# Performance work log

Measured on AMD Instinct MI355X. Metric: run time of the kernel, lower is better.

Reference implementation:

```python
import jax, jax.numpy as jnp
import numpy as np

# model constants
D = 2048; D_INNER = 4096; H = 64; P = 64; N = 128; K = 4; CHUNK = 256
E = 8; TOPK = 2; I_EXP = 1024; I_SH = 4096
EPS = 1e-5; RES_MULT = 0.22
CONV_DIM = D_INNER + 2 * N  # n_groups=1


def rmsnorm(x, w, eps=EPS):
    var = jnp.mean(x * x, axis=-1, keepdims=True)
    return x * jax.lax.rsqrt(var + eps) * w


def segsum(x):
    # x: [..., L] -> [..., L, L] lower-triangular cumulative sums, -inf above diag
    L = x.shape[-1]
    cs = jnp.cumsum(x, axis=-1)
    d = cs[..., :, None] - cs[..., None, :]
    mask = jnp.tril(jnp.ones((L, L), dtype=bool))
    return jnp.where(mask, d, -jnp.inf)


def ssd(x, dt, A, Bm, Cm, chunk=CHUNK):
    # x:[b,s,h,p] dt:[b,s,h] A:[h] Bm/Cm:[b,s,n] (single group)
    b, S, h, p = x.shape
    n = Bm.shape[-1]
    nc = S // chunk
    xc = x.reshape(b, nc, chunk, h, p)
    dtc = dt.reshape(b, nc, chunk, h)
    Bc = Bm.reshape(b, nc, chunk, n)
    Cc = Cm.reshape(b, nc, chunk, n)
    dA = jnp.transpose(dtc * A, (0, 1, 3, 2))          # [b,c,h,l]
    dA_cum = jnp.cumsum(dA, axis=-1)                    # [b,c,h,l]
    xdt = xc * dtc[..., None]                           # [b,c,l,h,p]
    # intra-chunk (quadratic attention-like block)
    CB = jnp.einsum('bcln,bcsn->bcls', Cc, Bc)
    Lmat = jnp.exp(segsum(dA))                          # [b,c,h,l,s]
    Y = jnp.einsum('bcls,bchls,bcshp->bclhp', CB, Lmat, xdt)
    # per-chunk final states
    decay_states = jnp.exp(dA_cum[..., -1:] - dA_cum)   # [b,c,h,l]
    states = jnp.einsum('bcln,bchl,bclhp->bchpn', Bc, decay_states, xdt)
    # inter-chunk recurrence (small scan over nc chunks)
    chunk_decay = jnp.exp(dA_cum[..., -1])              # [b,c,h]
    dec_c = jnp.moveaxis(chunk_decay, 1, 0)             # [c,b,h]
    st_c = jnp.moveaxis(states, 1, 0)                   # [c,b,h,p,n]

    def step(carry, inp):
        dec, st = inp
        return carry * dec[..., None, None] + st, carry

    _, prev = jax.lax.scan(step, jnp.zeros_like(st_c[0]), (dec_c, st_c))
    prev = jnp.moveaxis(prev, 0, 1)                     # [b,c,h,p,n] state before each chunk
    out_decay = jnp.exp(jnp.transpose(dA_cum, (0, 1, 3, 2)))  # [b,c,l,h]
    Y = Y + jnp.einsum('bcln,bchpn->bclhp', Cc, prev) * out_decay[..., None]
    return Y.reshape(b, S, h, p)


def causal_conv_silu(u, w, bias):
    # u:[b,s,c], depthwise causal conv kernel w:[c,K]
    S = u.shape[1]
    up = jnp.pad(u, ((0, 0), (K - 1, 0), (0, 0)))
    y = sum(up[:, i:i + S, :] * w[:, i] for i in range(K)) + bias
    return jax.nn.silu(y)


def setup_inputs() -> dict:
    key = jax.random.key(0)
    ks = jax.random.split(key, 16)
    B, S = 1, 4096
    sc = 0.02
    return {
        'positions': jnp.arange(B * S, dtype=jnp.int32).reshape(B, S),
        'hidden_states': jax.random.normal(ks[0], (B, S, D), jnp.float32),
        'ln1_w': jnp.ones((D,), jnp.float32),
        'in_proj_w': jax.random.normal(ks[1], (D, 2 * D_INNER + 2 * N + H), jnp.float32) * sc,
        'conv_w': jax.random.normal(ks[2], (CONV_DIM, K), jnp.float32) * 0.2,
        'conv_b': jnp.zeros((CONV_DIM,), jnp.float32),
        'A_log': jnp.log(jax.random.uniform(ks[3], (H,), jnp.float32, 1.0, 16.0)),
        'dt_bias': jax.random.normal(ks[4], (H,), jnp.float32) * 0.5,
        'D_param': jnp.ones((H,), jnp.float32),
        'mamba_norm_w': jnp.ones((D_INNER,), jnp.float32),
        'out_proj_w': jax.random.normal(ks[5], (D_INNER, D), jnp.float32) * sc,
        'ln2_w': jnp.ones((D,), jnp.float32),
        'router_w': jax.random.normal(ks[6], (D, E), jnp.float32) * sc,
        'moe_w_gate_up': jax.random.normal(ks[7], (E, D, 2 * I_EXP), jnp.float32) * sc,
        'moe_w_down': jax.random.normal(ks[8], (E, I_EXP, D), jnp.float32) * sc,
        'shared_w_in': jax.random.normal(ks[9], (D, 2 * I_SH), jnp.float32) * sc,
        'shared_w_out': jax.random.normal(ks[10], (I_SH, D), jnp.float32) * sc,
    }


def reference(positions, hidden_states, ln1_w, in_proj_w, conv_w, conv_b, A_log,
              dt_bias, D_param, mamba_norm_w, out_proj_w, ln2_w, router_w,
              moe_w_gate_up, moe_w_down, shared_w_in, shared_w_out):
    B, S, _ = hidden_states.shape
    residual = hidden_states
    h = rmsnorm(hidden_states, ln1_w)
    # ---- Mamba2 mixer ----
    proj = h @ in_proj_w                                  # [B,S,2*Di+2N+H]
    z = proj[..., :D_INNER]
    xBC = proj[..., D_INNER:D_INNER + CONV_DIM]
    dt_raw = proj[..., D_INNER + CONV_DIM:]
    xBC = causal_conv_silu(xBC, conv_w, conv_b)
    x = xBC[..., :D_INNER].reshape(B, S, H, P)
    Bm = xBC[..., D_INNER:D_INNER + N]
    Cm = xBC[..., D_INNER + N:]
    dt = jax.nn.softplus(dt_raw + dt_bias)                # [B,S,H]
    A = -jnp.exp(A_log)                                   # [H]
    y = ssd(x, dt, A, Bm, Cm) + x * D_param[None, None, :, None]
    y = y.reshape(B, S, D_INNER)
    y = rmsnorm(y * jax.nn.silu(z), mamba_norm_w)         # gated RMSNorm
    mamba_out = y @ out_proj_w
    hidden = residual + mamba_out * RES_MULT
    residual = hidden
    # ---- MoE + shared MLP ----
    h2 = rmsnorm(hidden, ln2_w)
    ht = h2.reshape(-1, D)
    T = ht.shape[0]
    logits = ht @ router_w                                # [T,E]
    topv, topi = jax.lax.top_k(logits, TOPK)
    wts = jax.nn.softmax(topv, axis=-1)
    gates = jnp.zeros((T, E), ht.dtype).at[jnp.arange(T)[:, None], topi].set(wts)
    moe_out = jnp.zeros_like(ht)
    for e in range(E):
        gu = ht @ moe_w_gate_up[e]
        a = jax.nn.silu(gu[:, :I_EXP]) * gu[:, I_EXP:]
        moe_out = moe_out + gates[:, e:e + 1] * (a @ moe_w_down[e])
    gu = ht @ shared_w_in
    shared_out = (jax.nn.silu(gu[:, :I_SH]) * gu[:, I_SH:]) @ shared_w_out
    ff = (moe_out + shared_out).reshape(B, S, D)
    hidden = residual + ff * RES_MULT
    return (hidden, residual)
```

## Files before the change

kernel.cpp:

```cpp
#include <hip/hip_runtime.h>
#include <stdint.h>

typedef unsigned short u16;
typedef __attribute__((ext_vector_type(8))) __bf16 bf16x8;
typedef __attribute__((ext_vector_type(4))) float f32x4;

#define SEQ     4096
#define DMODEL  2048
#define DINNER  4096
#define NHEADS  64
#define HEADP   64
#define NSTATE  128
#define NCHUNK  16
#define CHUNKL  256
#define NPROJ   8512
#define NPROJP  8576
#define CONVDIM 4352
#define RESM    0.22f
#define MAXROWS 9216
#define MAXTILE 72

static __device__ __forceinline__ u16 f2bf(float f){
  union { float f; uint32_t u; } v; v.f = f;
  uint32_t r = v.u + 0x7fffu + ((v.u >> 16) & 1u);
  return (u16)(r >> 16);
}
static __device__ __forceinline__ float bf2f(u16 h){
  union { uint32_t u; float f; } v; v.u = ((uint32_t)h) << 16;
  return v.f;
}
static __device__ __forceinline__ float siluf(float x){ return x / (1.f + __expf(-x)); }

static __device__ __forceinline__ void gll16(const void* g, void* l) {
  __builtin_amdgcn_global_load_lds(
      (const __attribute__((address_space(1))) void*)g,
      (__attribute__((address_space(3))) void*)l, 16, 0, 0);
}

static __device__ __forceinline__ void decode_tile(
    int id, int NB, int MB, int G, int& bx, int& by)
{
  const int nwg = NB * MB;
  int sid = id;
  if (!(nwg & 7)) {
    const int cpx = nwg >> 3;
    sid = (id & 7) * cpx + (id >> 3);
  }
  const int gsz = MB * G;
  const int fullG = NB / G;
  const int fullCnt = fullG * gsz;
  if (sid < fullCnt) {
    const int grp = sid / gsz;
    const int r = sid - grp * gsz;
    const int q = r / G;
    by = q;
    bx = grp * G + (r - q * G);
  } else {
    const int rem = NB - fullG * G;
    const int r = sid - fullCnt;
    const int q = r / rem;
    by = q;
    bx = fullG * G + (r - q * rem);
  }
}

__global__ __launch_bounds__(256) void rmsnorm_kernel(
    const float* __restrict__ in, const float* __restrict__ w,
    u16* __restrict__ out, int width)
{
  const int row = blockIdx.x;
  const float* x = in + (size_t)row * width;
  float ss = 0.f;
  for (int i = threadIdx.x * 4; i < width; i += 1024) {
    float4 v = *(const float4*)&x[i];
    ss += v.x*v.x + v.y*v.y + v.z*v.z + v.w*v.w;
  }
  #pragma unroll
  for (int off = 32; off > 0; off >>= 1) ss += __shfl_down(ss, off);
  __shared__ float red[4];
  if ((threadIdx.x & 63) == 0) red[threadIdx.x >> 6] = ss;
  __syncthreads();
  const float total = red[0] + red[1] + red[2] + red[3];
  const float scale = rsqrtf(total / (float)width + 1e-5f);
  u16* o = out + (size_t)row * width;
  for (int i = threadIdx.x * 4; i < width; i += 1024) {
    float4 v = *(const float4*)&x[i];
    float4 g = *(const float4*)&w[i];
    o[i+0] = f2bf(v.x * scale * g.x);
    o[i+1] = f2bf(v.y * scale * g.y);
    o[i+2] = f2bf(v.z * scale * g.z);
    o[i+3] = f2bf(v.w * scale * g.w);
  }
}

__global__ __launch_bounds__(256) void rmsnorm_split(
    const float* __restrict__ in, const float* __restrict__ w,
    u16* __restrict__ hi, u16* __restrict__ lo, int width)
{
  const int row = blockIdx.x;
  const float* x = in + (size_t)row * width;
  float ss = 0.f;
  for (int i = threadIdx.x * 4; i < width; i += 1024) {
    float4 v = *(const float4*)&x[i];
    ss += v.x*v.x + v.y*v.y + v.z*v.z + v.w*v.w;
  }
  #pragma unroll
  for (int off = 32; off > 0; off >>= 1) ss += __shfl_down(ss, off);
  __shared__ float red[4];
  if ((threadIdx.x & 63) == 0) red[threadIdx.x >> 6] = ss;
  __syncthreads();
  const float total = red[0] + red[1] + red[2] + red[3];
  const float scale = rsqrtf(total / (float)width + 1e-5f);
  u16* oh = hi + (size_t)row * width;
  u16* ol = lo + (size_t)row * width;
  for (int i = threadIdx.x * 4; i < width; i += 1024) {
    float4 v = *(const float4*)&x[i];
    float4 g = *(const float4*)&w[i];
    #pragma unroll
    for (int q = 0; q < 4; q++) {
      const float val = ((const float*)&v)[q] * scale * ((const float*)&g)[q];
      const u16 H = f2bf(val);
      oh[i+q] = H;
      ol[i+q] = f2bf(val - bf2f(H));
    }
  }
}

__global__ __launch_bounds__(256) void wconv_t(
    const float* __restrict__ W, u16* __restrict__ Bt, int K, int N)
{
  const size_t eo = (size_t)blockIdx.z * K * N;
  W += eo; Bt += eo;
  __shared__ float t[32][33];
  const int n0 = blockIdx.x * 32, k0 = blockIdx.y * 32;
  const int tx = threadIdx.x & 31, ty = threadIdx.x >> 5;
  #pragma unroll
  for (int r = 0; r < 32; r += 8)
    t[ty + r][tx] = W[(size_t)(k0 + ty + r) * N + n0 + tx];
  __syncthreads();
  #pragma unroll
  for (int r = 0; r < 32; r += 8)
    Bt[(size_t)(n0 + ty + r) * K + k0 + tx] = f2bf(t[tx][ty + r]);
}

__global__ __launch_bounds__(256) void wconv_t_split(
    const float* __restrict__ W, u16* __restrict__ Bth, u16* __restrict__ Btl, int K, int N)
{
  __shared__ float t[32][33];
  const int n0 = blockIdx.x * 32, k0 = blockIdx.y * 32;
  const int tx = threadIdx.x & 31, ty = threadIdx.x >> 5;
  #pragma unroll
  for (int r = 0; r < 32; r += 8)
    t[ty + r][tx] = W[(size_t)(k0 + ty + r) * N + n0 + tx];
  __syncthreads();
  #pragma unroll
  for (int r = 0; r < 32; r += 8) {
    const float val = t[tx][ty + r];
    const u16 H = f2bf(val);
    const size_t idx = (size_t)(n0 + ty + r) * K + k0 + tx;
    Bth[idx] = H;
    Btl[idx] = f2bf(val - bf2f(H));
  }
}

template<int EPI>
__global__ __launch_bounds__(256, 2) void gemm_bt(
    const u16* __restrict__ A, const u16* __restrict__ Bt,
    float* __restrict__ Cf,
    int Nreal, int K, int ldc, int NB, int MB, int G)
{
  __shared__ u16 As[128 * 32];
  __shared__ u16 Bs[128 * 32];
  int bx, by; decode_tile(blockIdx.x, NB, MB, G, bx, by);
  const int tid = threadIdx.x, lane = tid & 63;
  const int wid = tid >> 6, wr = wid >> 1, wc = wid & 1;
  const int m0 = by * 128, n0 = bx * 128;
  const int fr = lane & 15, g = lane >> 4;
  const f32x4 zero = {0.f, 0.f, 0.f, 0.f};
  f32x4 acc[4][4];
  #pragma unroll
  for (int i = 0; i < 4; i++)
    #pragma unroll
    for (int j = 0; j < 4; j++) acc[i][j] = zero;
  const u16* pA = A  + (size_t)(m0 + (tid >> 2)) * K + (tid & 3) * 8;
  const u16* pB = Bt + (size_t)(n0 + (tid >> 2)) * K + (tid & 3) * 8;
  const size_t rstep = (size_t)64 * K;
  const int l0 = tid * 8;
  for (int k0 = 0; k0 < K; k0 += 32) {
    if (k0) __syncthreads();
    gll16(pA + k0,         &As[l0]);
    gll16(pA + k0 + rstep, &As[2048 + l0]);
    gll16(pB + k0,         &Bs[l0]);
    gll16(pB + k0 + rstep, &Bs[2048 + l0]);
    __syncthreads();
    bf16x8 af[4], bfr[4];
    #pragma unroll
    for (int mi = 0; mi < 4; mi++)
      af[mi] = *(const bf16x8*)&As[(wr * 64 + mi * 16 + fr) * 32 + g * 8];
    #pragma unroll
    for (int ni = 0; ni < 4; ni++)
      bfr[ni] = *(const bf16x8*)&Bs[(wc * 64 + ni * 16 + fr) * 32 + g * 8];
    #pragma unroll
    for (int mi = 0; mi < 4; mi++)
      #pragma unroll
      for (int ni = 0; ni < 4; ni++)
        acc[mi][ni] = __builtin_amdgcn_mfma_f32_16x16x32_bf16(af[mi], bfr[ni], acc[mi][ni], 0, 0, 0);
  }
  #pragma unroll
  for (int mi = 0; mi < 4; mi++) {
    #pragma unroll
    for (int ni = 0; ni < 4; ni++) {
      const int n = n0 + wc * 64 + ni * 16 + fr;
      if (n >= Nreal) continue;
      #pragma unroll
      for (int i = 0; i < 4; i++) {
        const int m = m0 + wr * 64 + mi * 16 + g * 4 + i;
        Cf[(size_t)m * ldc + n] = acc[mi][ni][i];
      }
    }
  }
}

template<int EPI>
__global__ __launch_bounds__(256, 2) void gemm_dd(
    const u16* __restrict__ Ah, const u16* __restrict__ Al,
    const u16* __restrict__ Bh, const u16* __restrict__ Bl,
    float* __restrict__ Cf, const float* __restrict__ res,
    int Nreal, int K, int ldc, float alpha, int NB, int MB, int G)
{
  __shared__ u16 Ash[128 * 32];
  __shared__ u16 Asl[128 * 32];
  __shared__ u16 Bsh[128 * 32];
  __shared__ u16 Bsl[128 * 32];
  int bx, by; decode_tile(blockIdx.x, NB, MB, G, bx, by);
  const int tid = threadIdx.x, lane = tid & 63;
  const int wid = tid >> 6, wr = wid >> 1, wc = wid & 1;
  const int m0 = by * 128, n0 = bx * 128;
  const int fr = lane & 15, g = lane >> 4;
  const f32x4 zero = {0.f, 0.f, 0.f, 0.f};
  f32x4 acc[4][4];
  #pragma unroll
  for (int i = 0; i < 4; i++)
    #pragma unroll
    for (int j = 0; j < 4; j++) acc[i][j] = zero;
  const size_t offA = (size_t)(m0 + (tid >> 2)) * K + (tid & 3) * 8;
  const size_t offB = (size_t)(n0 + (tid >> 2)) * K + (tid & 3) * 8;
  const size_t rstep = (size_t)64 * K;
  const int l0 = tid * 8;
  for (int k0 = 0; k0 < K; k0 += 32) {
    if (k0) __syncthreads();
    gll16(Ah + offA + k0,         &Ash[l0]);
    gll16(Ah + offA + k0 + rstep, &Ash[2048 + l0]);
    gll16(Al + offA + k0,         &Asl[l0]);
    gll16(Al + offA + k0 + rstep, &Asl[2048 + l0]);
    gll16(Bh + offB + k0,         &Bsh[l0]);
    gll16(Bh + offB + k0 + rstep, &Bsh[2048 + l0]);
    gll16(Bl + offB + k0,         &Bsl[l0]);
    gll16(Bl + offB + k0 + rstep, &Bsl[2048 + l0]);
    __syncthreads();
    bf16x8 ah[4], al[4], bh[4], bl[4];
    #pragma unroll
    for (int mi = 0; mi < 4; mi++) {
      const int a = (wr * 64 + mi * 16 + fr) * 32 + g * 8;
      ah[mi] = *(const bf16x8*)&Ash[a];
      al[mi] = *(const bf16x8*)&Asl[a];
    }
    #pragma unroll
    for (int ni = 0; ni < 4; ni++) {
      const int b = (wc * 64 + ni * 16 + fr) * 32 + g * 8;
      bh[ni] = *(const bf16x8*)&Bsh[b];
      bl[ni] = *(const bf16x8*)&Bsl[b];
    }
    #pragma unroll
    for (int mi = 0; mi < 4; mi++)
      #pragma unroll
      for (int ni = 0; ni < 4; ni++) {
        acc[mi][ni] = __builtin_amdgcn_mfma_f32_16x16x32_bf16(al[mi], bh[ni], acc[mi][ni], 0, 0, 0);
        acc[mi][ni] = __builtin_amdgcn_mfma_f32_16x16x32_bf16(ah[mi], bl[ni], acc[mi][ni], 0, 0, 0);
        acc[mi][ni] = __builtin_amdgcn_mfma_f32_16x16x32_bf16(ah[mi], bh[ni], acc[mi][ni], 0, 0, 0);
      }
  }
  #pragma unroll
  for (int mi = 0; mi < 4; mi++) {
    #pragma unroll
    for (int ni = 0; ni < 4; ni++) {
      const int n = n0 + wc * 64 + ni * 16 + fr;
      if (n >= Nreal) continue;
      #pragma unroll
      for (int i = 0; i < 4; i++) {
        const int m = m0 + wr * 64 + mi * 16 + g * 4 + i;
        const float v = acc[mi][ni][i];
        const size_t idx = (size_t)m * ldc + n;
        if constexpr (EPI == 1) {
          Cf[idx] = res[idx] + alpha * v;
        } else {
          Cf[idx] = v;
        }
      }
    }
  }
}

__global__ __launch_bounds__(256, 2) void gemm_moe_gu(
    const u16* __restrict__ ht, const u16* __restrict__ wGU,
    float* __restrict__ guf, const int* __restrict__ tokmap,
    const int* __restrict__ meta)
{
  const int by = blockIdx.y;
  if (by >= meta[24]) return;
  const int e = meta[32 + by];
  const int row0 = meta[104 + by];
  __shared__ u16 As[128 * 32];
  __shared__ u16 Bs[128 * 32];
  const int tid = threadIdx.x, lane = tid & 63;
  const int wid = tid >> 6, wr = wid >> 1, wc = wid & 1;
  const int n0 = blockIdx.x * 128;
  const int fr = lane & 15, g = lane >> 4;
  const f32x4 zero = {0.f, 0.f, 0.f, 0.f};
  f32x4 acc[4][4];
  #pragma unroll
  for (int i = 0; i < 4; i++)
    #pragma unroll
    for (int j = 0; j < 4; j++) acc[i][j] = zero;
  const int r4 = tid >> 2, c8 = (tid & 3) * 8;
  const int tok0 = tokmap[row0 + r4];
  const int tok1 = tokmap[row0 + 64 + r4];
  const u16* pA0 = ht + (size_t)tok0 * DMODEL + c8;
  const u16* pA1 = ht + (size_t)tok1 * DMODEL + c8;
  const u16* pB  = wGU + (size_t)e * 2048 * DMODEL + (size_t)(n0 + r4) * DMODEL + c8;
  const size_t rstep = (size_t)64 * DMODEL;
  const int l0 = tid * 8;
  for (int k0 = 0; k0 < DMODEL; k0 += 32) {
    if (k0) __syncthreads();
    gll16(pA0 + k0,        &As[l0]);
    gll16(pA1 + k0,        &As[2048 + l0]);
    gll16(pB + k0,         &Bs[l0]);
    gll16(pB + k0 + rstep, &Bs[2048 + l0]);
    __syncthreads();
    bf16x8 af[4], bfr[4];
    #pragma unroll
    for (int mi = 0; mi < 4; mi++)
      af[mi] = *(const bf16x8*)&As[(wr * 64 + mi * 16 + fr) * 32 + g * 8];
    #pragma unroll
    for (int ni = 0; ni < 4; ni++)
      bfr[ni] = *(const bf16x8*)&Bs[(wc * 64 + ni * 16 + fr) * 32 + g * 8];
    #pragma unroll
    for (int mi = 0; mi < 4; mi++)
      #pragma unroll
      for (int ni = 0; ni < 4; ni++)
        acc[mi][ni] = __builtin_amdgcn_mfma_f32_16x16x32_bf16(af[mi], bfr[ni], acc[mi][ni], 0, 0, 0);
  }
  #pragma unroll
  for (int mi = 0; mi < 4; mi++)
    #pragma unroll
    for (int ni = 0; ni < 4; ni++) {
      const int n = n0 + wc * 64 + ni * 16 + fr;
      #pragma unroll
      for (int i = 0; i < 4; i++) {
        const int m = row0 + wr * 64 + mi * 16 + g * 4 + i;
        guf[(size_t)m * 2048 + n] = acc[mi][ni][i];
      }
    }
}

__global__ __launch_bounds__(256, 2) void gemm_moe_down(
    const u16* __restrict__ abuf, const u16* __restrict__ wDN,
    u16* __restrict__ dout, const float* __restrict__ gatew,
    const int* __restrict__ meta)
{
  const int by = blockIdx.y;
  if (by >= meta[24]) return;
  const int e = meta[32 + by];
  const int row0 = meta[104 + by];
  __shared__ u16 As[128 * 32];
  __shared__ u16 Bs[128 * 32];
  const int tid = threadIdx.x, lane = tid & 63;
  const int wid = tid >> 6, wr = wid >> 1, wc = wid & 1;
  const int n0 = blockIdx.x * 128;
  const int fr = lane & 15, g = lane >> 4;
  const f32x4 zero = {0.f, 0.f, 0.f, 0.f};
  f32x4 acc[4][4];
  #pragma unroll
  for (int i = 0; i < 4; i++)
    #pragma unroll
    for (int j = 0; j < 4; j++) acc[i][j] = zero;
  const int r4 = tid >> 2, c8 = (tid & 3) * 8;
  const u16* pA = abuf + (size_t)(row0 + r4) * 1024 + c8;
  const u16* pB = wDN + (size_t)e * 1024 * 2048 + (size_t)(n0 + r4) * 1024 + c8;
  const size_t rstepA = (size_t)64 * 1024;
  const int l0 = tid * 8;
  for (int k0 = 0; k0 < 1024; k0 += 32) {
    if (k0) __syncthreads();
    gll16(pA + k0,          &As[l0]);
    gll16(pA + k0 + rstepA, &As[2048 + l0]);
    gll16(pB + k0,          &Bs[l0]);
    gll16(pB + k0 + rstepA, &Bs[2048 + l0]);
    __syncthreads();
    bf16x8 af[4], bfr[4];
    #pragma unroll
    for (int mi = 0; mi < 4; mi++)
      af[mi] = *(const bf16x8*)&As[(wr * 64 + mi * 16 + fr) * 32 + g * 8];
    #pragma unroll
    for (int ni = 0; ni < 4; ni++)
      bfr[ni] = *(const bf16x8*)&Bs[(wc * 64 + ni * 16 + fr) * 32 + g * 8];
    #pragma unroll
    for (int mi = 0; mi < 4; mi++)
      #pragma unroll
      for (int ni = 0; ni < 4; ni++)
        acc[mi][ni] = __builtin_amdgcn_mfma_f32_16x16x32_bf16(af[mi], bfr[ni], acc[mi][ni], 0, 0, 0);
  }
  #pragma unroll
  for (int mi = 0; mi < 4; mi++)
    #pragma unroll
    for (int ni = 0; ni < 4; ni++) {
      const int n = n0 + wc * 64 + ni * 16 + fr;
      #pragma unroll
      for (int i = 0; i < 4; i++) {
        const int m = row0 + wr * 64 + mi * 16 + g * 4 + i;
        dout[(size_t)m * 2048 + n] = f2bf(acc[mi][ni][i] * gatew[m]);
      }
    }
}

__global__ __launch_bounds__(256) void conv_silu_kernel(
    const float* __restrict__ proj, const float* __restrict__ cw, const float* __restrict__ cb,
    float* __restrict__ x, float* __restrict__ Bc, float* __restrict__ Cc)
{
  const int c = blockIdx.x * 256 + threadIdx.x;
  const int s = blockIdx.y;
  const float4 w = *(const float4*)&cw[c * 4];
  float acc = cb[c];
  const float* pc = proj + (size_t)DINNER + c;
  if (s >= 3) acc += pc[(size_t)(s-3) * NPROJP] * w.x;
  if (s >= 2) acc += pc[(size_t)(s-2) * NPROJP] * w.y;
  if (s >= 1) acc += pc[(size_t)(s-1) * NPROJP] * w.z;
  acc += pc[(size_t)s * NPROJP] * w.w;
  const float v = siluf(acc);
  if (c < DINNER)                 x[(size_t)s * DINNER + c] = v;
  else if (c < DINNER + NSTATE)   Bc[(size_t)s * NSTATE + (c - DINNER)] = v;
  else                            Cc[(size_t)s * NSTATE + (c - DINNER - NSTATE)] = v;
}

__global__ __launch_bounds__(256) void dt_kernel(
    const float* __restrict__ proj, const float* __restrict__ dt_bias, float* __restrict__ dt)
{
  const int i = blockIdx.x * 256 + threadIdx.x;
  const int s = i >> 6, h = i & 63;
  const float v = proj[(size_t)s * NPROJP + (DINNER + CONVDIM) + h] + dt_bias[h];
  dt[i] = fmaxf(v, 0.f) + log1pf(__expf(-fabsf(v)));
}

__global__ __launch_bounds__(64) void ssd_cum_seq(
    const float* __restrict__ dt, const float* __restrict__ A_log,
    float* __restrict__ cum, float* __restrict__ cdec)
{
  const int c = blockIdx.x, h = threadIdx.x;
  const float A = -__expf(A_log[h]);
  float run = 0.f;
  float* co = cum + ((size_t)(c * 64 + h)) * 256;
  const float* dp = dt + (size_t)c * 256 * 64 + h;
  #pragma unroll 4
  for (int l = 0; l < 256; l++) {
    run += dp[(size_t)l * 64] * A;
    co[l] = run;
  }
  cdec[c * 64 + h] = __expf(run);
}

__global__ __launch_bounds__(256) void ssd_cb(
    const float* __restrict__ Cc, const float* __restrict__ Bc, float* __restrict__ CBt)
{
  const int c = blockIdx.y;
  const int lt = blockIdx.x >> 2, st = blockIdx.x & 3;
  if (st > lt) return;
  __shared__ float Cn[128][64];
  __shared__ float Bn[128][64];
  const int tid = threadIdx.x;
  #pragma unroll
  for (int rep = 0; rep < 8; rep++) {
    const int lin = rep * 1024 + tid * 4;
    const int r = lin >> 7, cc = lin & 127;
    float4 cv = *(const float4*)&Cc[((size_t)(c*256 + lt*64 + r)) * 128 + cc];
    float4 bv = *(const float4*)&Bc[((size_t)(c*256 + st*64 + r)) * 128 + cc];
    Cn[cc+0][r] = cv.x; Cn[cc+1][r] = cv.y; Cn[cc+2][r] = cv.z; Cn[cc+3][r] = cv.w;
    Bn[cc+0][r] = bv.x; Bn[cc+1][r] = bv.y; Bn[cc+2][r] = bv.z; Bn[cc+3][r] = bv.w;
  }
  __syncthreads();
  const int lb = (tid >> 4) * 4, sb = (tid & 15) * 4;
  float acc[4][4] = {};
  for (int n = 0; n < 128; n++) {
    float cv[4], bv[4];
    #pragma unroll
    for (int i = 0; i < 4; i++) { cv[i] = Cn[n][lb+i]; bv[i] = Bn[n][sb+i]; }
    #pragma unroll
    for (int i = 0; i < 4; i++)
      #pragma unroll
      for (int j = 0; j < 4; j++) acc[i][j] += cv[i] * bv[j];
  }
  #pragma unroll
  for (int is = 0; is < 4; is++) {
    const int sg = st*64 + sb + is;
    float4 o; o.x = acc[0][is]; o.y = acc[1][is]; o.z = acc[2][is]; o.w = acc[3][is];
    *(float4*)&CBt[((size_t)(c*256 + sg)) * 256 + lt*64 + lb] = o;
  }
}

__global__ __launch_bounds__(256, 2) void ssd_intra(
    const float* __restrict__ x, const float* __restrict__ dt, const float* __restrict__ cum,
    const float* __restrict__ CBt, float* __restrict__ Yw)
{
  const int c = blockIdx.x, h = blockIdx.y, l = threadIdx.x;
  __shared__ float xs[64][64];
  __shared__ float cumL[256];
  cumL[l] = cum[((size_t)(c*64 + h)) * 256 + l];
  float Y[64];
  #pragma unroll
  for (int p = 0; p < 64; p++) Y[p] = 0.f;
  const size_t cb0 = (size_t)c * 256 * 256;
  for (int st4 = 0; st4 < 4; st4++) {
    __syncthreads();
    {
      const int j = threadIdx.x >> 2, p0 = (threadIdx.x & 3) * 16;
      const int sg = c*256 + st4*64 + j;
      const float dtv = dt[(size_t)sg * 64 + h];
      const float* xr = x + (size_t)sg * DINNER + h*64 + p0;
      #pragma unroll
      for (int q4 = 0; q4 < 4; q4++) {
        const float4 v = *(const float4*)&xr[q4*4];
        xs[j][p0 + q4*4+0] = v.x * dtv;
        xs[j][p0 + q4*4+1] = v.y * dtv;
        xs[j][p0 + q4*4+2] = v.z * dtv;
        xs[j][p0 + q4*4+3] = v.w * dtv;
      }
    }
    __syncthreads();
    if (st4 * 64 <= l) {
      const float myc = cumL[l];
      const int smax = (64 < l - st4*64 + 1) ? 64 : (l - st4*64 + 1);
      for (int s = 0; s < smax; s++) {
        const int sg = st4*64 + s;
        const float coef = CBt[cb0 + (size_t)sg*256 + l] * __expf(myc - cumL[sg]);
        const float4* xr4 = (const float4*)&xs[s][0];
        #pragma unroll
        for (int p4 = 0; p4 < 16; p4++) {
          const float4 xv = xr4[p4];
          Y[p4*4+0] += coef * xv.x;
          Y[p4*4+1] += coef * xv.y;
          Y[p4*4+2] += coef * xv.z;
          Y[p4*4+3] += coef * xv.w;
        }
      }
    }
  }
  float* yo = Yw + (size_t)(c*256 + l) * DINNER + h*64;
  #pragma unroll
  for (int p4 = 0; p4 < 16; p4++) {
    float4 o; o.x = Y[p4*4+0]; o.y = Y[p4*4+1]; o.z = Y[p4*4+2]; o.w = Y[p4*4+3];
    *(float4*)&yo[p4*4] = o;
  }
}

__global__ __launch_bounds__(256, 2) void ssd_states(
    const float* __restrict__ x, const float* __restrict__ Bc, const float* __restrict__ dt,
    const float* __restrict__ cum, float* __restrict__ states)
{
  const int c = blockIdx.x, h = blockIdx.y;
  const int p = threadIdx.x >> 2, n0 = (threadIdx.x & 3) * 32;
  __shared__ float xl[64][64];
  __shared__ float Bl[64][128];
  __shared__ float cd[256];
  {
    const int l = threadIdx.x;
    const float* cumh = cum + ((size_t)(c*64 + h)) * 256;
    cd[l] = __expf(cumh[255] - cumh[l]) * dt[(size_t)(c*256 + l) * 64 + h];
  }
  float stv[32];
  #pragma unroll
  for (int q = 0; q < 32; q++) stv[q] = 0.f;
  for (int lt = 0; lt < 4; lt++) {
    __syncthreads();
    {
      const int j = threadIdx.x >> 2, p0 = (threadIdx.x & 3) * 16;
      const int sg = c*256 + lt*64 + j;
      const float* xr = x + (size_t)sg * DINNER + h*64 + p0;
      #pragma unroll
      for (int q4 = 0; q4 < 4; q4++)
        *(float4*)&xl[j][p0 + q4*4] = *(const float4*)&xr[q4*4];
    }
    #pragma unroll
    for (int rep = 0; rep < 8; rep++) {
      const int lin = rep * 1024 + threadIdx.x * 4;
      const int r = lin >> 7, cc = lin & 127;
      *(float4*)&Bl[r][cc] = *(const float4*)&Bc[((size_t)(c*256 + lt*64 + r)) * 128 + cc];
    }
    __syncthreads();
    for (int j = 0; j < 64; j++) {
      const float v = xl[j][p] * cd[lt*64 + j];
      const float4* br = (const float4*)&Bl[j][n0];
      #pragma unroll
      for (int q4 = 0; q4 < 8; q4++) {
        const float4 bv = br[q4];
        stv[q4*4+0] += v * bv.x;
        stv[q4*4+1] += v * bv.y;
        stv[q4*4+2] += v * bv.z;
        stv[q4*4+3] += v * bv.w;
      }
    }
  }
  float* so = states + (((size_t)(c*64 + h)) * 64 + p) * 128 + n0;
  #pragma unroll
  for (int q4 = 0; q4 < 8; q4++) {
    float4 o; o.x = stv[q4*4+0]; o.y = stv[q4*4+1]; o.z = stv[q4*4+2]; o.w = stv[q4*4+3];
    *(float4*)&so[q4*4] = o;
  }
}

__global__ void ssd_scan(
    const float* __restrict__ states, const float* __restrict__ cdec, float* __restrict__ prev)
{
  const int hp = blockIdx.x;
  const int n = threadIdx.x;
  const int h = hp >> 6;
  float carry = 0.f;
  for (int c = 0; c < NCHUNK; c++) {
    const size_t idx = ((size_t)c * 4096 + hp) * 128 + n;
    prev[idx] = carry;
    carry = carry * cdec[c*64 + h] + states[idx];
  }
}

__global__ __launch_bounds__(256, 2) void ssd_final(
    const float* __restrict__ Cc, const float* __restrict__ prev, const float* __restrict__ cum,
    const float* __restrict__ x, const float* __restrict__ proj, const float* __restrict__ Dp,
    float* __restrict__ Yw)
{
  const int c = blockIdx.x, h = blockIdx.y, l = threadIdx.x;
  __shared__ float pv[64][128];
  #pragma unroll
  for (int rep = 0; rep < 8; rep++) {
    const int lin = rep * 1024 + threadIdx.x * 4;
    const int p = lin >> 7, n = lin & 127;
    *(float4*)&pv[p][n] = *(const float4*)&prev[((size_t)c * 4096 + h*64 + p) * 128 + n];
  }
  __syncthreads();
  float acc[64];
  #pragma unroll
  for (int p = 0; p < 64; p++) acc[p] = 0.f;
  const float* ccrow = Cc + (size_t)(c*256 + l) * 128;
  for (int nt = 0; nt < 4; nt++) {
    float cr[32];
    #pragma unroll
    for (int j4 = 0; j4 < 8; j4++) {
      const float4 v = *(const float4*)&ccrow[nt*32 + j4*4];
      cr[j4*4+0] = v.x; cr[j4*4+1] = v.y; cr[j4*4+2] = v.z; cr[j4*4+3] = v.w;
    }
    #pragma unroll
    for (int p = 0; p < 64; p++) {
      const float4* pvp = (const float4*)&pv[p][nt*32];
      float s = 0.f;
      #pragma unroll
      for (int j4 = 0; j4 < 8; j4++) {
        const float4 b = pvp[j4];
        s += cr[j4*4+0]*b.x + cr[j4*4+1]*b.y + cr[j4*4+2]*b.z + cr[j4*4+3]*b.w;
      }
      acc[p] += s;
    }
  }
  const float odec = __expf(cum[((size_t)(c*64 + h)) * 256 + l]);
  const float Dv = Dp[h];
  const float* xr = x + (size_t)(c*256 + l) * DINNER + h*64;
  const float* zr = proj + (size_t)(c*256 + l) * NPROJP + h*64;
  float* yo = Yw + (size_t)(c*256 + l) * DINNER + h*64;
  #pragma unroll
  for (int p = 0; p < 64; p++) {
    const float yv = yo[p] + acc[p] * odec + Dv * xr[p];
    yo[p] = yv * siluf(zr[p]);
  }
}

__global__ __launch_bounds__(256) void router_kernel(
    const float* __restrict__ h2, const float* __restrict__ ln2w,
    const float* __restrict__ rw, int* __restrict__ eidx, float* __restrict__ ew)
{
  const int t = blockIdx.x;
  const float* xr = h2 + (size_t)t * DMODEL;
  float ss = 0.f;
  for (int i = threadIdx.x; i < DMODEL; i += 256) { const float v = xr[i]; ss += v*v; }
  #pragma unroll
  for (int off = 32; off > 0; off >>= 1) ss += __shfl_down(ss, off);
  __shared__ float red[4];
  if ((threadIdx.x & 63) == 0) red[threadIdx.x >> 6] = ss;
  __syncthreads();
  const float scale = rsqrtf((red[0]+red[1]+red[2]+red[3]) / (float)DMODEL + 1e-5f);
  float acc[8];
  #pragma unroll
  for (int j = 0; j < 8; j++) acc[j] = 0.f;
  for (int i = threadIdx.x; i < DMODEL; i += 256) {
    const float v = xr[i] * scale * ln2w[i];
    const float* r = rw + (size_t)i * 8;
    #pragma unroll
    for (int j = 0; j < 8; j++) acc[j] += v * r[j];
  }
  #pragma unroll
  for (int j = 0; j < 8; j++)
    #pragma unroll
    for (int off = 32; off > 0; off >>= 1) acc[j] += __shfl_down(acc[j], off);
  __shared__ float rbuf[4][8];
  if ((threadIdx.x & 63) == 0)
    #pragma unroll
    for (int j = 0; j < 8; j++) rbuf[threadIdx.x >> 6][j] = acc[j];
  __syncthreads();
  if (threadIdx.x == 0) {
    float lg[8];
    #pragma unroll
    for (int j = 0; j < 8; j++) lg[j] = rbuf[0][j]+rbuf[1][j]+rbuf[2][j]+rbuf[3][j];
    int i1 = 0;
    #pragma unroll
    for (int j = 1; j < 8; j++) if (lg[j] > lg[i1]) i1 = j;
    int i2 = -1;
    #pragma unroll
    for (int j = 0; j < 8; j++) if (j != i1 && (i2 < 0 || lg[j] > lg[i2])) i2 = j;
    const float e2 = __expf(lg[i2] - lg[i1]);
    const float inv = 1.f / (1.f + e2);
    eidx[t*2]   = i1;  ew[t*2]   = inv;
    eidx[t*2+1] = i2;  ew[t*2+1] = e2 * inv;
  }
}

__global__ void moe_zero(int* __restrict__ tokmap, int* __restrict__ meta)
{
  const int i = blockIdx.x * 256 + threadIdx.x;
  if (i < MAXROWS) tokmap[i] = 0;
  if (i < 16) meta[i] = 0;
}

__global__ void moe_count(const int* __restrict__ eidx, int* __restrict__ meta)
{
  const int i = blockIdx.x * 256 + threadIdx.x;
  if (i < SEQ * 2) atomicAdd(&meta[eidx[i]], 1);
}

__global__ void moe_offsets(int* __restrict__ meta)
{
  if (threadIdx.x != 0 || blockIdx.x != 0) return;
  int off = 0, T = 0;
  for (int e = 0; e < 8; e++) {
    meta[16 + e] = off;
    const int nt = (meta[e] + 127) >> 7;
    for (int j = 0; j < nt; j++) {
      meta[32 + T] = e;
      meta[104 + T] = off + j * 128;
      T++;
    }
    off += nt * 128;
  }
  meta[24] = T;
}

__global__ void moe_place(
    const int* __restrict__ eidx, const float* __restrict__ ew,
    int* __restrict__ meta, int* __restrict__ tokmap,
    float* __restrict__ gatew, int* __restrict__ posmap)
{
  const int i = blockIdx.x * 256 + threadIdx.x;
  if (i >= SEQ * 2) return;
  const int e = eidx[i];
  const int pos = atomicAdd(&meta[8 + e], 1);
  const int r = meta[16 + e] + pos;
  tokmap[r] = i >> 1;
  gatew[r] = ew[i];
  posmap[i] = r;
}

__global__ __launch_bounds__(256) void glu_kernel(
    const float* __restrict__ gu, u16* __restrict__ a, int I)
{
  const int i = blockIdx.x * 256 + threadIdx.x;
  const int t = blockIdx.y;
  const float lv = gu[(size_t)t * 2 * I + i];
  const float rv = gu[(size_t)t * 2 * I + I + i];
  a[(size_t)t * I + i] = f2bf(siluf(lv) * rv);
}

__global__ __launch_bounds__(256) void final_moe(
    const float* __restrict__ h2, const float* __restrict__ shout,
    const u16* __restrict__ dout, const int* __restrict__ posmap,
    float* __restrict__ o)
{
  const int t = blockIdx.x;
  const int p0 = posmap[t*2], p1 = posmap[t*2+1];
  const u16* d0 = dout + (size_t)p0 * 2048 + threadIdx.x * 8;
  const u16* d1 = dout + (size_t)p1 * 2048 + threadIdx.x * 8;
  const size_t base = (size_t)t * 2048 + threadIdx.x * 8;
  #pragma unroll
  for (int q = 0; q < 8; q++) {
    const float ff = shout[base + q] + bf2f(d0[q]) + bf2f(d1[q]);
    o[base + q] = h2[base + q] + RESM * ff;
  }
}

#define OFF_WAH   ((size_t)0)
#define OFF_WAL   ((size_t)35127296)
#define OFF_PROJ  ((size_t)70254592)
#define OFF_X     ((size_t)210763776)
#define OFF_Y     ((size_t)277872640)
#define OFF_HP    ((size_t)344981504)
#define OFF_BC    ((size_t)378535936)
#define OFF_CC    ((size_t)380633088)
#define OFF_DT    ((size_t)382730240)
#define OFF_CUM   ((size_t)383778816)
#define OFF_CDEC  ((size_t)384827392)
#define OFF_CB    ((size_t)384831488)

extern "C" void kernel_launch(void* const* d_in, const int* in_sizes, int n_in,
                              void* d_out, int out_size, void* d_ws, size_t ws_size,
                              hipStream_t stream)
{
  const float* hs       = (const float*)d_in[1];
  const float* ln1_w    = (const float*)d_in[2];
  const float* w_inproj = (const float*)d_in[3];
  const float* conv_w   = (const float*)d_in[4];
  const float* conv_b   = (const float*)d_in[5];
  const float* A_log    = (const float*)d_in[6];
  const float* dt_bias  = (const float*)d_in[7];
  const float* D_param  = (const float*)d_in[8];
  const float* mnorm_w  = (const float*)d_in[9];
  const float* w_outp   = (const float*)d_in[10];
  const float* ln2_w    = (const float*)d_in[11];
  const float* router_w = (const float*)d_in[12];
  const float* w_gu     = (const float*)d_in[13];
  const float* w_down   = (const float*)d_in[14];
  const float* w_shin   = (const float*)d_in[15];
  const float* w_shout  = (const float*)d_in[16];

  char* ws = (char*)d_ws;
  u16*   wAh    = (u16*)(ws + OFF_WAH);
  u16*   wAl    = (u16*)(ws + OFF_WAL);
  float* projf  = (float*)(ws + OFF_PROJ);
  float* xbuf   = (float*)(ws + OFF_X);
  float* ybuf   = (float*)(ws + OFF_Y);
  float* Bcb    = (float*)(ws + OFF_BC);
  float* Ccb    = (float*)(ws + OFF_CC);
  float* dtb    = (float*)(ws + OFF_DT);
  float* cumb   = (float*)(ws + OFF_CUM);
  float* cdecb  = (float*)(ws + OFF_CDEC);
  float* cbt    = (float*)(ws + OFF_CB);

  u16*   hhi    = (u16*)(ws + OFF_HP);
  u16*   hlo    = (u16*)(ws + OFF_HP + 16777216);
  float* prevb  = (float*)(ws + OFF_HP);
  u16*   wDN    = (u16*)(ws + OFF_HP);
  float* stbuf  = (float*)(ws + OFF_WAH);
  u16*   ynhi   = (u16*)(ws + OFF_WAH);
  u16*   ynlo   = (u16*)(ws + OFF_WAL);
  u16*   wBh    = (u16*)(ws + OFF_PROJ);
  u16*   wBl    = (u16*)(ws + OFF_PROJ + 16777216);
  u16*   wE     = (u16*)(ws + OFF_WAH);
  u16*   wD     = (u16*)(ws + OFF_WAH + 33554432);
  u16*   wGU    = (u16*)(ws + OFF_WAH);
  float* guf    = (float*)(ws + OFF_PROJ);
  u16*   abufp  = (u16*)(ws + OFF_PROJ + 83886080);
  u16*   ht     = (u16*)(ws + OFF_X);
  u16*   ash    = (u16*)(ws + OFF_X + 16777216);
  u16*   dout   = (u16*)(ws + OFF_X + 16777216);
  float* shout  = (float*)(ws + OFF_Y);

  int*   eidx   = (int*)(ws + OFF_BC);
  float* ew     = (float*)(ws + OFF_BC + 65536);
  int*   posmap = (int*)(ws + OFF_BC + 131072);
  int*   tokmap = (int*)(ws + OFF_BC + 196608);
  float* gatew  = (float*)(ws + OFF_BC + 262144);
  int*   meta   = (int*)(ws + OFF_BC + 327680);

  float* out0    = (float*)d_out;
  float* hidden2 = out0 + (size_t)SEQ * DMODEL;

  rmsnorm_split<<<SEQ, 256, 0, stream>>>(hs, ln1_w, hhi, hlo, DMODEL);
  wconv_t_split<<<dim3(NPROJ/32, DMODEL/32), 256, 0, stream>>>(w_inproj, wAh, wAl, DMODEL, NPROJ);
  gemm_dd<3><<<67*32, 256, 0, stream>>>(hhi, hlo, wAh, wAl, projf, nullptr,
                                        NPROJ, DMODEL, NPROJP, 0.f, 67, 32, 2);
  conv_silu_kernel<<<dim3(17, SEQ), 256, 0, stream>>>(projf, conv_w, conv_b, xbuf, Bcb, Ccb);
  dt_kernel<<<SEQ*NHEADS/256, 256, 0, stream>>>(projf, dt_bias, dtb);
  ssd_cum_seq<<<NCHUNK, 64, 0, stream>>>(dtb, A_log, cumb, cdecb);
  ssd_cb<<<dim3(16, NCHUNK), 256, 0, stream>>>(Ccb, Bcb, cbt);
  ssd_intra<<<dim3(NCHUNK, NHEADS), 256, 0, stream>>>(xbuf, dtb, cumb, cbt, ybuf);
  ssd_states<<<dim3(NCHUNK, NHEADS), 256, 0, stream>>>(xbuf, Bcb, dtb, cumb, stbuf);
  ssd_scan<<<NHEADS*HEADP, 128, 0, stream>>>(stbuf, cdecb, prevb);
  ssd_final<<<dim3(NCHUNK, NHEADS), 256, 0, stream>>>(Ccb, prevb, cumb, xbuf, projf, D_param, ybuf);
  rmsnorm_split<<<SEQ, 256, 0, stream>>>(ybuf, mnorm_w, ynhi, ynlo, DINNER);
  wconv_t_split<<<dim3(DMODEL/32, DINNER/32), 256, 0, stream>>>(w_outp, wBh, wBl, DINNER, DMODEL);
  gemm_dd<1><<<16*32, 256, 0, stream>>>(ynhi, ynlo, wBh, wBl, hidden2, hs,
                                        DMODEL, DINNER, DMODEL, RESM, 16, 32, 2);

  router_kernel<<<SEQ, 256, 0, stream>>>(hidden2, ln2_w, router_w, eidx, ew);
  rmsnorm_kernel<<<SEQ, 256, 0, stream>>>(hidden2, ln2_w, ht, DMODEL);
  moe_zero<<<(MAXROWS+255)/256, 256, 0, stream>>>(tokmap, meta);
  moe_count<<<SEQ*2/256, 256, 0, stream>>>(eidx, meta);
  moe_offsets<<<1, 64, 0, stream>>>(meta);
  moe_place<<<SEQ*2/256, 256, 0, stream>>>(eidx, ew, meta, tokmap, gatew, posmap);

  wconv_t<<<dim3(8192/32, DMODEL/32), 256, 0, stream>>>(w_shin, wE, DMODEL, 8192);
  gemm_bt<3><<<64*32, 256, 0, stream>>>(ht, wE, guf, 8192, DMODEL, 8192, 64, 32, 4);
  glu_kernel<<<dim3(16, SEQ), 256, 0, stream>>>(guf, ash, 4096);
  wconv_t<<<dim3(DMODEL/32, 4096/32), 256, 0, stream>>>(w_shout, wD, 4096, DMODEL);
  gemm_bt<3><<<16*32, 256, 0, stream>>>(ash, wD, shout, DMODEL, 4096, DMODEL, 16, 32, 4);

  wconv_t<<<dim3(2048/32, DMODEL/32, 8), 256, 0, stream>>>(w_gu, wGU, DMODEL, 2048);
  wconv_t<<<dim3(DMODEL/32, 1024/32, 8), 256, 0, stream>>>(w_down, wDN, 1024, DMODEL);
  gemm_moe_gu<<<dim3(16, MAXTILE), 256, 0, stream>>>(ht, wGU, guf, tokmap, meta);
  glu_kernel<<<dim3(4, MAXROWS), 256, 0, stream>>>(guf, abufp, 1024);
  gemm_moe_down<<<dim3(16, MAXTILE), 256, 0, stream>>>(abufp, wDN, dout, gatew, meta);

  final_moe<<<SEQ, 256, 0, stream>>>(hidden2, shout, dout, posmap, out0);
}
```

Baseline: 2.068 ms.

## Fuse GLU into gate-up GEMM epilogues via interleaved weight layout, merge small kernels

Gate and up weight columns are interleaved during the transpose-convert so that each gate/up pair lands in adjacent MFMA lanes. The shared and MoE gate-up GEMM epilogues can then apply silu(gate)*up with a lane shuffle and write bf16 directly. This removes the fp32 intermediate buffer and the separate GLU kernels. The change also merges conv+dt and router+rmsnorm into single kernels and raises the tile-grouping factor for the dense GEMMs. Half the epilogue lanes now sit idle on stores, and the bf16 stores are strided.

```diff
diff --git a/kernel.cpp b/kernel.cpp
--- a/kernel.cpp
+++ b/kernel.cpp
@@ -64,35 +64,6 @@
   }
 }
 
-__global__ __launch_bounds__(256) void rmsnorm_kernel(
-    const float* __restrict__ in, const float* __restrict__ w,
-    u16* __restrict__ out, int width)
-{
-  const int row = blockIdx.x;
-  const float* x = in + (size_t)row * width;
-  float ss = 0.f;
-  for (int i = threadIdx.x * 4; i < width; i += 1024) {
-    float4 v = *(const float4*)&x[i];
-    ss += v.x*v.x + v.y*v.y + v.z*v.z + v.w*v.w;
-  }
-  #pragma unroll
-  for (int off = 32; off > 0; off >>= 1) ss += __shfl_down(ss, off);
-  __shared__ float red[4];
-  if ((threadIdx.x & 63) == 0) red[threadIdx.x >> 6] = ss;
-  __syncthreads();
-  const float total = red[0] + red[1] + red[2] + red[3];
-  const float scale = rsqrtf(total / (float)width + 1e-5f);
-  u16* o = out + (size_t)row * width;
-  for (int i = threadIdx.x * 4; i < width; i += 1024) {
-    float4 v = *(const float4*)&x[i];
-    float4 g = *(const float4*)&w[i];
-    o[i+0] = f2bf(v.x * scale * g.x);
-    o[i+1] = f2bf(v.y * scale * g.y);
-    o[i+2] = f2bf(v.z * scale * g.z);
-    o[i+3] = f2bf(v.w * scale * g.w);
-  }
-}
-
 __global__ __launch_bounds__(256) void rmsnorm_split(
     const float* __restrict__ in, const float* __restrict__ w,
     u16* __restrict__ hi, u16* __restrict__ lo, int width)
@@ -141,6 +112,26 @@
   #pragma unroll
   for (int r = 0; r < 32; r += 8)
     Bt[(size_t)(n0 + ty + r) * K + k0 + tx] = f2bf(t[tx][ty + r]);
+}
+
+__global__ __launch_bounds__(256) void wconv_t_glu(
+    const float* __restrict__ W, u16* __restrict__ Bt, int K, int N, int H)
+{
+  const size_t eo = (size_t)blockIdx.z * K * N;
+  W += eo; Bt += eo;
+  __shared__ float t[32][33];
+  const int n0 = blockIdx.x * 32, k0 = blockIdx.y * 32;
+  const int tx = threadIdx.x & 31, ty = threadIdx.x >> 5;
+  #pragma unroll
+  for (int r = 0; r < 32; r += 8)
+    t[ty + r][tx] = W[(size_t)(k0 + ty + r) * N + n0 + tx];
+  __syncthreads();
+  #pragma unroll
+  for (int r = 0; r < 32; r += 8) {
+    const int n = n0 + ty + r;
+    const int orow = (n < H) ? (2 * n) : (2 * (n - H) + 1);
+    Bt[(size_t)orow * K + k0 + tx] = f2bf(t[tx][ty + r]);
+  }
 }
 
 __global__ __launch_bounds__(256) void wconv_t_split(
@@ -216,6 +207,66 @@
       for (int i = 0; i < 4; i++) {
         const int m = m0 + wr * 64 + mi * 16 + g * 4 + i;
         Cf[(size_t)m * ldc + n] = acc[mi][ni][i];
+      }
+    }
+  }
+}
+
+__global__ __launch_bounds__(256, 2) void gemm_bt_glu(
+    const u16* __restrict__ A, const u16* __restrict__ Bt,
+    u16* __restrict__ aout,
+    int K, int Nhalf, int NB, int MB, int G)
+{
+  __shared__ u16 As[128 * 32];
+  __shared__ u16 Bs[128 * 32];
+  int bx, by; decode_tile(blockIdx.x, NB, MB, G, bx, by);
+  const int tid = threadIdx.x, lane = tid & 63;
+  const int wid = tid >> 6, wr = wid >> 1, wc = wid & 1;
+  const int m0 = by * 128, n0 = bx * 128;
+  const int fr = lane & 15, g = lane >> 4;
+  const f32x4 zero = {0.f, 0.f, 0.f, 0.f};
+  f32x4 acc[4][4];
+  #pragma unroll
+  for (int i = 0; i < 4; i++)
+    #pragma unroll
+    for (int j = 0; j < 4; j++) acc[i][j] = zero;
+  const u16* pA = A  + (size_t)(m0 + (tid >> 2)) * K + (tid & 3) * 8;
+  const u16* pB = Bt + (size_t)(n0 + (tid >> 2)) * K + (tid & 3) * 8;
+  const size_t rstep = (size_t)64 * K;
+  const int l0 = tid * 8;
+  for (int k0 = 0; k0 < K; k0 += 32) {
+    if (k0) __syncthreads();
+    gll16(pA + k0,         &As[l0]);
+    gll16(pA + k0 + rstep, &As[2048 + l0]);
+    gll16(pB + k0,         &Bs[l0]);
+    gll16(pB + k0 + rstep, &Bs[2048 + l0]);
+    __syncthreads();
+    bf16x8 af[4], bfr[4];
+    #pragma unroll
+    for (int mi = 0; mi < 4; mi++)
+      af[mi] = *(const bf16x8*)&As[(wr * 64 + mi * 16 + fr) * 32 + g * 8];
+    #pragma unroll
+    for (int ni = 0; ni < 4; ni++)
+      bfr[ni] = *(const bf16x8*)&Bs[(wc * 64 + ni * 16 + fr) * 32 + g * 8];
+    #pragma unroll
+    for (int mi = 0; mi < 4; mi++)
+      #pragma unroll
+      for (int ni = 0; ni < 4; ni++)
+        acc[mi][ni] = __builtin_amdgcn_mfma_f32_16x16x32_bf16(af[mi], bfr[ni], acc[mi][ni], 0, 0, 0);
+  }
+  #pragma unroll
+  for (int mi = 0; mi < 4; mi++) {
+    #pragma unroll
+    for (int ni = 0; ni < 4; ni++) {
+      const int n = n0 + wc * 64 + ni * 16 + fr;
+      #pragma unroll
+      for (int i = 0; i < 4; i++) {
+        const float v = acc[mi][ni][i];
+        const float vp = __shfl_xor(v, 1);
+        if (!(fr & 1)) {
+          const int m = m0 + wr * 64 + mi * 16 + g * 4 + i;
+          aout[(size_t)m * Nhalf + (n >> 1)] = f2bf(siluf(v) * vp);
+        }
       }
     }
   }
@@ -303,7 +354,7 @@
 
 __global__ __launch_bounds__(256, 2) void gemm_moe_gu(
     const u16* __restrict__ ht, const u16* __restrict__ wGU,
-    float* __restrict__ guf, const int* __restrict__ tokmap,
+    u16* __restrict__ abufp, const int* __restrict__ tokmap,
     const int* __restrict__ meta)
 {
   const int by = blockIdx.y;
@@ -357,8 +408,12 @@
       const int n = n0 + wc * 64 + ni * 16 + fr;
       #pragma unroll
       for (int i = 0; i < 4; i++) {
-        const int m = row0 + wr * 64 + mi * 16 + g * 4 + i;
-        guf[(size_t)m * 2048 + n] = acc[mi][ni][i];
+        const float v = acc[mi][ni][i];
+        const float vp = __shfl_xor(v, 1);
+        if (!(fr & 1)) {
+          const int m = row0 + wr * 64 + mi * 16 + g * 4 + i;
+          abufp[(size_t)m * 1024 + (n >> 1)] = f2bf(siluf(v) * vp);
+        }
       }
     }
 }
@@ -422,32 +477,31 @@
     }
 }
 
-__global__ __launch_bounds__(256) void conv_silu_kernel(
+__global__ __launch_bounds__(256) void conv_silu_dt(
     const float* __restrict__ proj, const float* __restrict__ cw, const float* __restrict__ cb,
-    float* __restrict__ x, float* __restrict__ Bc, float* __restrict__ Cc)
+    const float* __restrict__ dt_bias,
+    float* __restrict__ x, float* __restrict__ Bc, float* __restrict__ Cc,
+    float* __restrict__ dt)
 {
   const int c = blockIdx.x * 256 + threadIdx.x;
   const int s = blockIdx.y;
-  const float4 w = *(const float4*)&cw[c * 4];
-  float acc = cb[c];
-  const float* pc = proj + (size_t)DINNER + c;
-  if (s >= 3) acc += pc[(size_t)(s-3) * NPROJP] * w.x;
-  if (s >= 2) acc += pc[(size_t)(s-2) * NPROJP] * w.y;
-  if (s >= 1) acc += pc[(size_t)(s-1) * NPROJP] * w.z;
-  acc += pc[(size_t)s * NPROJP] * w.w;
-  const float v = siluf(acc);
-  if (c < DINNER)                 x[(size_t)s * DINNER + c] = v;
-  else if (c < DINNER + NSTATE)   Bc[(size_t)s * NSTATE + (c - DINNER)] = v;
-  else                            Cc[(size_t)s * NSTATE + (c - DINNER - NSTATE)] = v;
-}
-
-__global__ __launch_bounds__(256) void dt_kernel(
-    const float* __restrict__ proj, const float* __restrict__ dt_bias, float* __restrict__ dt)
-{
-  const int i = blockIdx.x * 256 + threadIdx.x;
-  const int s = i >> 6, h = i & 63;
-  const float v = proj[(size_t)s * NPROJP + (DINNER + CONVDIM) + h] + dt_bias[h];
-  dt[i] = fmaxf(v, 0.f) + log1pf(__expf(-fabsf(v)));
+  if (c < CONVDIM) {
+    const float4 w = *(const float4*)&cw[c * 4];
+    float acc = cb[c];
+    const float* pc = proj + (size_t)DINNER + c;
+    if (s >= 3) acc += pc[(size_t)(s-3) * NPROJP] * w.x;
+    if (s >= 2) acc += pc[(size_t)(s-2) * NPROJP] * w.y;
+    if (s >= 1) acc += pc[(size_t)(s-1) * NPROJP] * w.z;
+    acc += pc[(size_t)s * NPROJP] * w.w;
+    const float v = siluf(acc);
+    if (c < DINNER)                 x[(size_t)s * DINNER + c] = v;
+    else if (c < DINNER + NSTATE)   Bc[(size_t)s * NSTATE + (c - DINNER)] = v;
+    else                            Cc[(size_t)s * NSTATE + (c - DINNER - NSTATE)] = v;
+  } else if (c < CONVDIM + 64) {
+    const int h = c - CONVDIM;
+    const float v = proj[(size_t)s * NPROJP + (DINNER + CONVDIM) + h] + dt_bias[h];
+    dt[(size_t)s * 64 + h] = fmaxf(v, 0.f) + log1pf(__expf(-fabsf(v)));
+  }
 }
 
 __global__ __launch_bounds__(64) void ssd_cum_seq(
@@ -678,14 +732,18 @@
   }
 }
 
-__global__ __launch_bounds__(256) void router_kernel(
+__global__ __launch_bounds__(256) void router_norm(
     const float* __restrict__ h2, const float* __restrict__ ln2w,
-    const float* __restrict__ rw, int* __restrict__ eidx, float* __restrict__ ew)
+    const float* __restrict__ rw, u16* __restrict__ ht,
+    int* __restrict__ eidx, float* __restrict__ ew)
 {
   const int t = blockIdx.x;
   const float* xr = h2 + (size_t)t * DMODEL;
   float ss = 0.f;
-  for (int i = threadIdx.x; i < DMODEL; i += 256) { const float v = xr[i]; ss += v*v; }
+  for (int i = threadIdx.x * 4; i < DMODEL; i += 1024) {
+    float4 v = *(const float4*)&xr[i];
+    ss += v.x*v.x + v.y*v.y + v.z*v.z + v.w*v.w;
+  }
   #pragma unroll
   for (int off = 32; off > 0; off >>= 1) ss += __shfl_down(ss, off);
   __shared__ float red[4];
@@ -695,8 +753,10 @@
   float acc[8];
   #pragma unroll
   for (int j = 0; j < 8; j++) acc[j] = 0.f;
+  u16* o = ht + (size_t)t * DMODEL;
   for (int i = threadIdx.x; i < DMODEL; i += 256) {
     const float v = xr[i] * scale * ln2w[i];
+    o[i] = f2bf(v);
     const float* r = rw + (size_t)i * 8;
     #pragma unroll
     for (int j = 0; j < 8; j++) acc[j] += v * r[j];
@@ -770,16 +830,6 @@
   tokmap[r] = i >> 1;
   gatew[r] = ew[i];
   posmap[i] = r;
-}
-
-__global__ __launch_bounds__(256) void glu_kernel(
-    const float* __restrict__ gu, u16* __restrict__ a, int I)
-{
-  const int i = blockIdx.x * 256 + threadIdx.x;
-  const int t = blockIdx.y;
-  const float lv = gu[(size_t)t * 2 * I + i];
-  const float rv = gu[(size_t)t * 2 * I + I + i];
-  a[(size_t)t * I + i] = f2bf(siluf(lv) * rv);
 }
 
 __global__ __launch_bounds__(256) void final_moe(
@@ -858,7 +908,6 @@
   u16*   wE     = (u16*)(ws + OFF_WAH);
   u16*   wD     = (u16*)(ws + OFF_WAH + 33554432);
   u16*   wGU    = (u16*)(ws + OFF_WAH);
-  float* guf    = (float*)(ws + OFF_PROJ);
   u16*   abufp  = (u16*)(ws + OFF_PROJ + 83886080);
   u16*   ht     = (u16*)(ws + OFF_X);
   u16*   ash    = (u16*)(ws + OFF_X + 16777216);
@@ -878,9 +927,9 @@
   rmsnorm_split<<<SEQ, 256, 0, stream>>>(hs, ln1_w, hhi, hlo, DMODEL);
   wconv_t_split<<<dim3(NPROJ/32, DMODEL/32), 256, 0, stream>>>(w_inproj, wAh, wAl, DMODEL, NPROJ);
   gemm_dd<3><<<67*32, 256, 0, stream>>>(hhi, hlo, wAh, wAl, projf, nullptr,
-                                        NPROJ, DMODEL, NPROJP, 0.f, 67, 32, 2);
-  conv_silu_kernel<<<dim3(17, SEQ), 256, 0, stream>>>(projf, conv_w, conv_b, xbuf, Bcb, Ccb);
-  dt_kernel<<<SEQ*NHEADS/256, 256, 0, stream>>>(projf, dt_bias, dtb);
+                                        NPROJ, DMODEL, NPROJP, 0.f, 67, 32, 4);
+  conv_silu_dt<<<dim3(18, SEQ), 256, 0, stream>>>(projf, conv_w, conv_b, dt_bias,
+                                                  xbuf, Bcb, Ccb, dtb);
   ssd_cum_seq<<<NCHUNK, 64, 0, stream>>>(dtb, A_log, cumb, cdecb);
   ssd_cb<<<dim3(16, NCHUNK), 256, 0, stream>>>(Ccb, Bcb, cbt);
   ssd_intra<<<dim3(NCHUNK, NHEADS), 256, 0, stream>>>(xbuf, dtb, cumb, cbt, ybuf);
@@ -890,25 +939,22 @@
   rmsnorm_split<<<SEQ, 256, 0, stream>>>(ybuf, mnorm_w, ynhi, ynlo, DINNER);
   wconv_t_split<<<dim3(DMODEL/32, DINNER/32), 256, 0, stream>>>(w_outp, wBh, wBl, DINNER, DMODEL);
   gemm_dd<1><<<16*32, 256, 0, stream>>>(ynhi, ynlo, wBh, wBl, hidden2, hs,
-                                        DMODEL, DINNER, DMODEL, RESM, 16, 32, 2);
-
-  router_kernel<<<SEQ, 256, 0, stream>>>(hidden2, ln2_w, router_w, eidx, ew);
-  rmsnorm_kernel<<<SEQ, 256, 0, stream>>>(hidden2, ln2_w, ht, DMODEL);
+                                        DMODEL, DINNER, DMODEL, RESM, 16, 32, 4);
+
+  router_norm<<<SEQ, 256, 0, stream>>>(hidden2, ln2_w, router_w, ht, eidx, ew);
   moe_zero<<<(MAXROWS+255)/256, 256, 0, stream>>>(tokmap, meta);
   moe_count<<<SEQ*2/256, 256, 0, stream>>>(eidx, meta);
   moe_offsets<<<1, 64, 0, stream>>>(meta);
   moe_place<<<SEQ*2/256, 256, 0, stream>>>(eidx, ew, meta, tokmap, gatew, posmap);
 
-  wconv_t<<<dim3(8192/32, DMODEL/32), 256, 0, stream>>>(w_shin, wE, DMODEL, 8192);
-  gemm_bt<3><<<64*32, 256, 0, stream>>>(ht, wE, guf, 8192, DMODEL, 8192, 64, 32, 4);
-  glu_kernel<<<dim3(16, SEQ), 256, 0, stream>>>(guf, ash, 4096);
+  wconv_t_glu<<<dim3(8192/32, DMODEL/32), 256, 0, stream>>>(w_shin, wE, DMODEL, 8192, 4096);
+  gemm_bt_glu<<<64*32, 256, 0, stream>>>(ht, wE, ash, DMODEL, 4096, 64, 32, 4);
   wconv_t<<<dim3(DMODEL/32, 4096/32), 256, 0, stream>>>(w_shout, wD, 4096, DMODEL);
   gemm_bt<3><<<16*32, 256, 0, stream>>>(ash, wD, shout, DMODEL, 4096, DMODEL, 16, 32, 4);
 
-  wconv_t<<<dim3(2048/32, DMODEL/32, 8), 256, 0, stream>>>(w_gu, wGU, DMODEL, 2048);
+  wconv_t_glu<<<dim3(2048/32, DMODEL/32, 8), 256, 0, stream>>>(w_gu, wGU, DMODEL, 2048, 1024);
   wconv_t<<<dim3(DMODEL/32, 1024/32, 8), 256, 0, stream>>>(w_down, wDN, 1024, DMODEL);
-  gemm_moe_gu<<<dim3(16, MAXTILE), 256, 0, stream>>>(ht, wGU, guf, tokmap, meta);
-  glu_kernel<<<dim3(4, MAXROWS), 256, 0, stream>>>(guf, abufp, 1024);
+  gemm_moe_gu<<<dim3(16, MAXTILE), 256, 0, stream>>>(ht, wGU, abufp, tokmap, meta);
   gemm_moe_down<<<dim3(16, MAXTILE), 256, 0, stream>>>(abufp, wDN, dout, gatew, meta);
 
   final_moe<<<SEQ, 256, 0, stream>>>(hidden2, shout, dout, posmap, out0);
```

Result: no change. 2.051 ms (-0.9%).
